# Kernel optimization log

Measured on AMD Instinct MI355X. Metric: run time of the kernel, lower is better.

The kernel has to match this reference:

```python
import jax, jax.numpy as jnp
import numpy as np

B, T, TS, J, D, H = 4, 512, 512, 17, 256, 8
CD = D // H
SCALE = CD ** -0.5


def setup_inputs() -> dict:
    key = jax.random.key(0)
    ks = jax.random.split(key, 7)
    return {
        "q": jax.random.normal(ks[0], (B, T, J, D), dtype=jnp.float32),
        "kv": jax.random.normal(ks[1], (B, TS, J, D), dtype=jnp.float32),
        "Wq": jax.random.normal(ks[2], (D, D), dtype=jnp.float32) * (D ** -0.5),
        "Wk": jax.random.normal(ks[3], (D, D), dtype=jnp.float32) * (D ** -0.5),
        "Wv": jax.random.normal(ks[4], (D, D), dtype=jnp.float32) * (D ** -0.5),
        "Wp": jax.random.normal(ks[5], (D, D), dtype=jnp.float32) * (D ** -0.5),
        "bp": jnp.zeros((D,), dtype=jnp.float32),
    }


def reference(q, kv, Wq, Wk, Wv, Wp, bp):
    b, t, j, d = q.shape
    t_sup = kv.shape[1]
    h, cd = H, CD
    # linear projections (torch Linear: x @ W^T), split heads -> [b,h,j,t,cd]
    qh = (q @ Wq.T).reshape(b, t, j, h, cd).transpose(0, 3, 2, 1, 4)
    kh = (kv @ Wk.T).reshape(b, t_sup, j, h, cd).transpose(0, 3, 2, 1, 4)
    vh = (kv @ Wv.T).reshape(b, t_sup, j, h, cd).transpose(0, 3, 2, 1, 4)
    # full attention matrix over temporal axes: [b,h,j,t,t_sup]
    scores = jnp.einsum("bhjtc,bhjsc->bhjts", qh, kh) * SCALE
    attn = jax.nn.softmax(scores, axis=-1)
    out = jnp.einsum("bhjts,bhjsc->bhjtc", attn, vh)
    out = out.transpose(0, 3, 2, 1, 4).reshape(b, t, j, d)  # [b,t,j,d]
    return out @ Wp.T + bp
```

## Files before the change

### kernel.cpp

```cpp
#include <hip/hip_runtime.h>
#include <hip/hip_bf16.h>

#define BB 4
#define TT 512
#define JJ 17
#define DD 256
#define HH 8
#define MROWS (BB*TT*JJ)
#define SZE ((size_t)MROWS * DD)
#define WSZ (DD*DD)
#define QSCALE 0.2550265247510319f
#define RST (17*256)

typedef short v8s __attribute__((ext_vector_type(8)));
typedef float v4f __attribute__((ext_vector_type(4)));
typedef float v16f __attribute__((ext_vector_type(16)));

__device__ __forceinline__ unsigned short f2bf(float f) {
    union { float f; unsigned int u; } c; c.f = f;
    unsigned int u = c.u;
    return (unsigned short)((u + 0x7FFF + ((u >> 16) & 1)) >> 16);
}
__device__ __forceinline__ unsigned int pkbf(float lo, float hi) {
    union { float f; unsigned int u; } a, b; a.f = lo; b.f = hi;
    return __builtin_amdgcn_perm(b.u + 0x8000u, a.u + 0x8000u, 0x07060302u);
}
__device__ __forceinline__ float fexp2(float x) {
    return __builtin_amdgcn_exp2f(x);
}

__device__ __forceinline__ void gld16(const unsigned short* g, unsigned short* l) {
    __builtin_amdgcn_global_load_lds(
        (const __attribute__((address_space(1))) void*)g,
        (__attribute__((address_space(3))) void*)l,
        16, 0, 0);
}

__global__ __launch_bounds__(256) void prepw_kernel(
    const float* __restrict__ Wq, const float* __restrict__ Wk,
    const float* __restrict__ Wv, const float* __restrict__ Wp,
    unsigned short* __restrict__ Wqb, unsigned short* __restrict__ Wkb,
    unsigned short* __restrict__ Wvb, unsigned short* __restrict__ Wpb)
{
    size_t k = ((size_t)blockIdx.x * 256 + threadIdx.x) * 8;
    int w = (int)(k >> 16);
    size_t off = k & (WSZ - 1);
    const float* src = (w == 0) ? Wq : (w == 1) ? Wk : (w == 2) ? Wv : Wp;
    unsigned short* dst = (w == 0) ? Wqb : (w == 1) ? Wkb : (w == 2) ? Wvb : Wpb;
    float4 x0 = *(const float4*)(src + off);
    float4 x1 = *(const float4*)(src + off + 4);
    union { unsigned short s[8]; int4 v; } u;
    u.s[0] = f2bf(x0.x); u.s[1] = f2bf(x0.y);
    u.s[2] = f2bf(x0.z); u.s[3] = f2bf(x0.w);
    u.s[4] = f2bf(x1.x); u.s[5] = f2bf(x1.y);
    u.s[6] = f2bf(x1.z); u.s[7] = f2bf(x1.w);
    *(int4*)(dst + off) = u.v;
}

__global__ __launch_bounds__(512) void gemm_kernel(
    const float* __restrict__ Aq,
    const float* __restrict__ Akv,
    const unsigned short* __restrict__ W0,
    const unsigned short* __restrict__ W1,
    const unsigned short* __restrict__ W2,
    unsigned short* __restrict__ Y0,
    unsigned short* __restrict__ Y1,
    unsigned short* __restrict__ Y2)
{
    const int z = blockIdx.y;
    const float* A          = (z == 0) ? Aq : Akv;
    const float ascale      = (z == 0) ? QSCALE : 1.f;
    const unsigned short* W = (z == 0) ? W0 : (z == 1) ? W1 : W2;
    unsigned short* Y       = (z == 0) ? Y0 : (z == 1) ? Y1 : Y2;

    const int bm = blockIdx.x;

    __shared__ unsigned short As[2][128 * 32];
    __shared__ unsigned short Bs[2][256 * 32];

    const int tid  = threadIdx.x;
    const int wv   = tid >> 6;
    const int lane = tid & 63;
    const int wm   = wv & 1;
    const int wn   = wv >> 1;
    const int quad = lane >> 4;
    const int l16  = lane & 15;

    const int srow  = tid >> 2;
    const int chunk = tid & 3;
    const int s4    = srow & 15;
    const int cg    = chunk ^ ((s4 ^ (s4 >> 2)) & 3);
    const float* gA = A + (size_t)(bm * 128 + srow) * 256 + cg * 8;
    const unsigned short* gB0 = W + (size_t)srow * 256 + cg * 8;
    const unsigned short* gB1 = W + (size_t)(128 + srow) * 256 + cg * 8;
    unsigned short* lA  = &As[0][tid * 8];
    unsigned short* lB0 = &Bs[0][tid * 8];
    unsigned short* lB1 = &Bs[0][4096 + tid * 8];

    const int rch8 = (quad ^ ((l16 ^ (l16 >> 2)) & 3)) * 8;

    v4f acc[4][4] = {};

    {
        float4 a0 = *(const float4*)(gA);
        float4 a1 = *(const float4*)(gA + 4);
        union { unsigned short s[8]; int4 v; } ua;
        ua.s[0] = f2bf(a0.x * ascale); ua.s[1] = f2bf(a0.y * ascale);
        ua.s[2] = f2bf(a0.z * ascale); ua.s[3] = f2bf(a0.w * ascale);
        ua.s[4] = f2bf(a1.x * ascale); ua.s[5] = f2bf(a1.y * ascale);
        ua.s[6] = f2bf(a1.z * ascale); ua.s[7] = f2bf(a1.w * ascale);
        *(int4*)(lA) = ua.v;
    }
    gld16(gB0, lB0);
    gld16(gB1, lB1);
    __syncthreads();

    for (int kt = 0; kt < 8; ++kt) {
        const int cur = kt & 1;
        const int nb  = cur ^ 1;
        float4 a0, a1;
        if (kt < 7) {
            const int nk = (kt + 1) * 32;
            a0 = *(const float4*)(gA + nk);
            a1 = *(const float4*)(gA + nk + 4);
            gld16(gB0 + nk, lB0 + nb * 8192);
            gld16(gB1 + nk, lB1 + nb * 8192);
        }
        v8s a[4], b[4];
        #pragma unroll
        for (int i = 0; i < 4; ++i)
            a[i] = *(const v8s*)(&As[cur][(wm * 64 + i * 16 + l16) * 32 + rch8]);
        #pragma unroll
        for (int j = 0; j < 4; ++j)
            b[j] = *(const v8s*)(&Bs[cur][(wn * 64 + j * 16 + l16) * 32 + rch8]);
        #pragma unroll
        for (int i = 0; i < 4; ++i)
            #pragma unroll
            for (int j = 0; j < 4; ++j)
                acc[i][j] = __builtin_amdgcn_mfma_f32_16x16x32_bf16(
                    a[i], b[j], acc[i][j], 0, 0, 0);
        if (kt < 7) {
            union { unsigned short s[8]; int4 v; } ua;
            ua.s[0] = f2bf(a0.x * ascale); ua.s[1] = f2bf(a0.y * ascale);
            ua.s[2] = f2bf(a0.z * ascale); ua.s[3] = f2bf(a0.w * ascale);
            ua.s[4] = f2bf(a1.x * ascale); ua.s[5] = f2bf(a1.y * ascale);
            ua.s[6] = f2bf(a1.z * ascale); ua.s[7] = f2bf(a1.w * ascale);
            *(int4*)(lA + nb * 4096) = ua.v;
        }
        __syncthreads();
    }

    #pragma unroll
    for (int i = 0; i < 4; ++i)
        #pragma unroll
        for (int j = 0; j < 4; ++j)
            #pragma unroll
            for (int r = 0; r < 4; ++r) {
                int gm = bm * 128 + wm * 64 + i * 16 + quad * 4 + r;
                int gn = wn * 64 + j * 16 + l16;
                Y[(size_t)gm * 256 + gn] = f2bf(acc[i][j][r]);
            }
}

__global__ __launch_bounds__(256) void gemmo_kernel(
    const unsigned short* __restrict__ A,
    const unsigned short* __restrict__ W,
    const float* __restrict__ bias,
    float* __restrict__ out)
{
    const int bm = blockIdx.x;

    __shared__ unsigned short As[2][64 * 32];
    __shared__ unsigned short Bs[2][256 * 32];

    const int tid  = threadIdx.x;
    const int lane = tid & 63;
    const int wn   = tid >> 6;
    const int quad = lane >> 4;
    const int l16  = lane & 15;

    const int arow  = tid >> 2;
    const int chunk = tid & 3;
    const int cgA   = (chunk ^ ((arow ^ (arow >> 2)) & 3)) * 8;
    const unsigned short* gA = A + (size_t)(bm * 64 + arow) * 256 + cgA;
    const unsigned short* gB = W + (size_t)arow * 256 + cgA;
    unsigned short* lA = &As[0][tid * 8];
    unsigned short* lB = &Bs[0][tid * 8];

    const int rch8 = (quad ^ ((l16 ^ (l16 >> 2)) & 3)) * 8;

    v4f acc[4][4] = {};

    gld16(gA, lA);
    #pragma unroll
    for (int p = 0; p < 4; ++p)
        gld16(gB + (size_t)p * 64 * 256, lB + p * 2048);
    __syncthreads();

    for (int kt = 0; kt < 8; ++kt) {
        const int cur = kt & 1;
        if (kt < 7) {
            const int nk = (kt + 1) * 32;
            const int nb = cur ^ 1;
            gld16(gA + nk, lA + nb * 2048);
            #pragma unroll
            for (int p = 0; p < 4; ++p)
                gld16(gB + (size_t)p * 64 * 256 + nk, lB + nb * 8192 + p * 2048);
        }
        v8s a[4], b[4];
        #pragma unroll
        for (int i = 0; i < 4; ++i)
            a[i] = *(const v8s*)(&As[cur][(i * 16 + l16) * 32 + rch8]);
        #pragma unroll
        for (int j = 0; j < 4; ++j)
            b[j] = *(const v8s*)(&Bs[cur][(wn * 64 + j * 16 + l16) * 32 + rch8]);
        #pragma unroll
        for (int i = 0; i < 4; ++i)
            #pragma unroll
            for (int j = 0; j < 4; ++j)
                acc[i][j] = __builtin_amdgcn_mfma_f32_16x16x32_bf16(
                    a[i], b[j], acc[i][j], 0, 0, 0);
        __syncthreads();
    }

    #pragma unroll
    for (int i = 0; i < 4; ++i)
        #pragma unroll
        for (int j = 0; j < 4; ++j)
            #pragma unroll
            for (int r = 0; r < 4; ++r) {
                int gm = bm * 64 + i * 16 + quad * 4 + r;
                int gn = wn * 64 + j * 16 + l16;
                out[(size_t)gm * 256 + gn] = acc[i][j][r] + bias[gn];
            }
}

#define VST 136

__global__ __launch_bounds__(256, 4) void attn_kernel(
    const unsigned short* __restrict__ Qp,
    const unsigned short* __restrict__ Kp,
    const unsigned short* __restrict__ Vp,
    unsigned short* __restrict__ Att)
{
    const int id  = blockIdx.x;
    const int bjh = (id & 7) | ((id >> 5) << 3);
    const int qt  = (id >> 3) & 3;
    const int h   = bjh & 7;
    const int bj  = bjh >> 3;
    const int j   = bj % 17;
    const int b_  = bj / 17;

    __shared__ unsigned short Ks[128 * 40];
    __shared__ unsigned short Vs[32 * VST];
    __shared__ float Ls[128];

    const int tid  = threadIdx.x;
    const int wave = tid >> 6;
    const int lane = tid & 63;
    const int quad = lane >> 4;
    const int l16  = lane & 15;
    const int qo   = quad & 1;
    const int q2   = quad >> 1;

    const int base0 = b_ * 512 * RST + j * 256 + h * 32;

    v8s qa[2];
    #pragma unroll
    for (int fi = 0; fi < 2; ++fi)
        qa[fi] = *(const v8s*)(
            Qp + base0 + (qt * 128 + wave * 32 + fi * 16 + l16) * RST + quad * 8);

    float lacc[2] = {0.f, 0.f};
    v16f accO = {};

    for (int kc = 0; kc < 4; ++kc) {
        __syncthreads();
        #pragma unroll
        for (int c = 0; c < 2; ++c) {
            int krow = wave * 16 + l16 + c * 64;
            *(int4*)(&Ks[krow * 40 + quad * 8]) = *(const int4*)(
                Kp + base0 + (kc * 128 + krow) * RST + quad * 8);
        }
        #pragma unroll
        for (int c = 0; c < 2; ++c) {
            int idx  = c * 256 + tid;
            int srow = idx >> 2;
            int cd0  = (idx & 3) << 3;
            int xof  = (((srow >> 3) ^ (cd0 >> 3)) << 3) + (srow & 7);
            union { int4 v; unsigned short s[8]; } u;
            u.v = *(const int4*)(
                Vp + base0 + (kc * 128 + srow) * RST + cd0);
            #pragma unroll
            for (int i = 0; i < 8; ++i)
                Vs[(cd0 + i) * VST + xof] = u.s[i];
        }
        __syncthreads();

        #pragma unroll
        for (int half = 0; half < 2; ++half) {
            #pragma unroll
            for (int si = 0; si < 4; ++si) {
                v8s kb = *(const v8s*)(&Ks[((half * 4 + si) * 16 + l16) * 40 + quad * 8]);
                v4f st0 = {}, st1 = {};
                __builtin_amdgcn_s_setprio(1);
                st0 = __builtin_amdgcn_mfma_f32_16x16x32_bf16(kb, qa[0], st0, 0, 0, 0);
                st1 = __builtin_amdgcn_mfma_f32_16x16x32_bf16(kb, qa[1], st1, 0, 0, 0);
                __builtin_amdgcn_s_setprio(0);
                float p00 = fexp2(st0[0]), p01 = fexp2(st0[1]);
                float p02 = fexp2(st0[2]), p03 = fexp2(st0[3]);
                float p10 = fexp2(st1[0]), p11 = fexp2(st1[1]);
                float p12 = fexp2(st1[2]), p13 = fexp2(st1[3]);
                lacc[0] += (p00 + p01) + (p02 + p03);
                lacc[1] += (p10 + p11) + (p12 + p13);
                unsigned int D00 = pkbf(p00, p01), D01 = pkbf(p02, p03);
                unsigned int D10 = pkbf(p10, p11), D11 = pkbf(p12, p13);
                unsigned int P0 = qo ? D00 : D10;
                unsigned int P1 = qo ? D01 : D11;
                unsigned int S0 = __shfl_xor(P0, 16);
                unsigned int S1 = __shfl_xor(P1, 16);
                union { unsigned int u[4]; v8s v; } pa;
                pa.u[0] = qo ? S0 : D00;
                pa.u[1] = qo ? S1 : D01;
                pa.u[2] = qo ? D10 : S0;
                pa.u[3] = qo ? D11 : S1;
                int cd   = qo * 16 + l16;
                int sblk = half * 8 + si * 2 + q2;
                v8s vb = *(const v8s*)(&Vs[cd * VST + ((sblk ^ (cd >> 3)) << 3)]);
                __builtin_amdgcn_s_setprio(1);
                accO = __builtin_amdgcn_mfma_f32_32x32x16_bf16(pa.v, vb, accO, 0, 0, 0);
                __builtin_amdgcn_s_setprio(0);
            }
        }
    }

    #pragma unroll
    for (int fi = 0; fi < 2; ++fi) {
        float lv = lacc[fi];
        lv += __shfl_xor(lv, 16);
        lv += __shfl_xor(lv, 32);
        if (quad == 0) Ls[wave * 32 + fi * 16 + l16] = lv;
    }
    asm volatile("s_waitcnt lgkmcnt(0)" ::: "memory");

    const int cdo = qo * 16 + l16;
    #pragma unroll
    for (int g = 0; g < 4; ++g) {
        float4 lv = *(float4*)(&Ls[wave * 32 + g * 8 + q2 * 4]);
        float rl[4] = {1.f / lv.x, 1.f / lv.y, 1.f / lv.z, 1.f / lv.w};
        #pragma unroll
        for (int r = 0; r < 4; ++r) {
            int qrow = g * 8 + q2 * 4 + r;
            int trow = qt * 128 + wave * 32 + qrow;
            float v  = accO[g * 4 + r] * rl[r];
            Att[(size_t)(base0 + trow * RST + cdo)] = f2bf(v);
        }
    }
}

extern "C" void kernel_launch(void* const* d_in, const int* in_sizes, int n_in,
                              void* d_out, int out_size, void* d_ws, size_t ws_size,
                              hipStream_t stream) {
    const float* q  = (const float*)d_in[0];
    const float* kv = (const float*)d_in[1];
    const float* Wq = (const float*)d_in[2];
    const float* Wk = (const float*)d_in[3];
    const float* Wv = (const float*)d_in[4];
    const float* Wp = (const float*)d_in[5];
    const float* bp = (const float*)d_in[6];

    unsigned short* ws  = (unsigned short*)d_ws;
    unsigned short* Qp  = ws;
    unsigned short* Kp  = ws + SZE;
    unsigned short* Vp  = ws + 2 * SZE;
    unsigned short* Att = ws + 3 * SZE;
    unsigned short* Wqb = ws + 4 * SZE;
    unsigned short* Wkb = Wqb + WSZ;
    unsigned short* Wvb = Wkb + WSZ;
    unsigned short* Wpb = Wvb + WSZ;
    float* out = (float*)d_out;

    prepw_kernel<<<128, 256, 0, stream>>>(Wq, Wk, Wv, Wp,
                                          Wqb, Wkb, Wvb, Wpb);
    gemm_kernel<<<dim3(272, 3), 512, 0, stream>>>(
        q, kv, Wqb, Wkb, Wvb, Qp, Kp, Vp);
    attn_kernel<<<dim3(2176), 256, 0, stream>>>(Qp, Kp, Vp, Att);
    gemmo_kernel<<<dim3(544), 256, 0, stream>>>(Att, Wpb, bp, out);
}
```

Baseline: 198.6 us.

## Drop LDS staging in projection GEMMs and load MFMA operands directly from global

Both projection GEMM kernels stop staging tiles through double-buffered shared memory with async global-to-LDS loads and barriers. Each wave now reads its MFMA operand fragments straight from global memory, relying on the L1/L2 caches for reuse across waves. The QKV GEMM also shrinks to 64-row tiles with 256 threads, doubling the grid. This removes LDS traffic and synchronisation but gives up explicit prefetch and adds redundant global/cache reads, since the A rows are now loaded by all four waves and converted four times.

```diff
diff --git a/kernel.cpp b/kernel.cpp
--- a/kernel.cpp
+++ b/kernel.cpp
@@ -27,13 +27,6 @@
 }
 __device__ __forceinline__ float fexp2(float x) {
     return __builtin_amdgcn_exp2f(x);
-}
-
-__device__ __forceinline__ void gld16(const unsigned short* g, unsigned short* l) {
-    __builtin_amdgcn_global_load_lds(
-        (const __attribute__((address_space(1))) void*)g,
-        (__attribute__((address_space(3))) void*)l,
-        16, 0, 0);
 }
 
 __global__ __launch_bounds__(256) void prepw_kernel(
@@ -57,7 +50,7 @@
     *(int4*)(dst + off) = u.v;
 }
 
-__global__ __launch_bounds__(512) void gemm_kernel(
+__global__ __launch_bounds__(256) void gemm_kernel(
     const float* __restrict__ Aq,
     const float* __restrict__ Akv,
     const unsigned short* __restrict__ W0,
@@ -73,81 +66,42 @@
     const unsigned short* W = (z == 0) ? W0 : (z == 1) ? W1 : W2;
     unsigned short* Y       = (z == 0) ? Y0 : (z == 1) ? Y1 : Y2;
 
-    const int bm = blockIdx.x;
-
-    __shared__ unsigned short As[2][128 * 32];
-    __shared__ unsigned short Bs[2][256 * 32];
-
+    const int bm   = blockIdx.x;
     const int tid  = threadIdx.x;
-    const int wv   = tid >> 6;
+    const int wn   = tid >> 6;
     const int lane = tid & 63;
-    const int wm   = wv & 1;
-    const int wn   = wv >> 1;
     const int quad = lane >> 4;
     const int l16  = lane & 15;
 
-    const int srow  = tid >> 2;
-    const int chunk = tid & 3;
-    const int s4    = srow & 15;
-    const int cg    = chunk ^ ((s4 ^ (s4 >> 2)) & 3);
-    const float* gA = A + (size_t)(bm * 128 + srow) * 256 + cg * 8;
-    const unsigned short* gB0 = W + (size_t)srow * 256 + cg * 8;
-    const unsigned short* gB1 = W + (size_t)(128 + srow) * 256 + cg * 8;
-    unsigned short* lA  = &As[0][tid * 8];
-    unsigned short* lB0 = &Bs[0][tid * 8];
-    unsigned short* lB1 = &Bs[0][4096 + tid * 8];
-
-    const int rch8 = (quad ^ ((l16 ^ (l16 >> 2)) & 3)) * 8;
+    const float*          ga = A + (size_t)(bm * 64 + l16) * 256 + quad * 8;
+    const unsigned short* gb = W + (size_t)(wn * 64 + l16) * 256 + quad * 8;
 
     v4f acc[4][4] = {};
 
-    {
-        float4 a0 = *(const float4*)(gA);
-        float4 a1 = *(const float4*)(gA + 4);
-        union { unsigned short s[8]; int4 v; } ua;
-        ua.s[0] = f2bf(a0.x * ascale); ua.s[1] = f2bf(a0.y * ascale);
-        ua.s[2] = f2bf(a0.z * ascale); ua.s[3] = f2bf(a0.w * ascale);
-        ua.s[4] = f2bf(a1.x * ascale); ua.s[5] = f2bf(a1.y * ascale);
-        ua.s[6] = f2bf(a1.z * ascale); ua.s[7] = f2bf(a1.w * ascale);
-        *(int4*)(lA) = ua.v;
-    }
-    gld16(gB0, lB0);
-    gld16(gB1, lB1);
-    __syncthreads();
-
+    #pragma unroll 2
     for (int kt = 0; kt < 8; ++kt) {
-        const int cur = kt & 1;
-        const int nb  = cur ^ 1;
-        float4 a0, a1;
-        if (kt < 7) {
-            const int nk = (kt + 1) * 32;
-            a0 = *(const float4*)(gA + nk);
-            a1 = *(const float4*)(gA + nk + 4);
-            gld16(gB0 + nk, lB0 + nb * 8192);
-            gld16(gB1 + nk, lB1 + nb * 8192);
-        }
+        const int k0 = kt * 32;
         v8s a[4], b[4];
         #pragma unroll
-        for (int i = 0; i < 4; ++i)
-            a[i] = *(const v8s*)(&As[cur][(wm * 64 + i * 16 + l16) * 32 + rch8]);
+        for (int i = 0; i < 4; ++i) {
+            float4 x0 = *(const float4*)(ga + i * 16 * 256 + k0);
+            float4 x1 = *(const float4*)(ga + i * 16 * 256 + k0 + 4);
+            union { unsigned short s[8]; v8s v; } ua;
+            ua.s[0] = f2bf(x0.x * ascale); ua.s[1] = f2bf(x0.y * ascale);
+            ua.s[2] = f2bf(x0.z * ascale); ua.s[3] = f2bf(x0.w * ascale);
+            ua.s[4] = f2bf(x1.x * ascale); ua.s[5] = f2bf(x1.y * ascale);
+            ua.s[6] = f2bf(x1.z * ascale); ua.s[7] = f2bf(x1.w * ascale);
+            a[i] = ua.v;
+        }
         #pragma unroll
         for (int j = 0; j < 4; ++j)
-            b[j] = *(const v8s*)(&Bs[cur][(wn * 64 + j * 16 + l16) * 32 + rch8]);
+            b[j] = *(const v8s*)(gb + (size_t)j * 16 * 256 + k0);
         #pragma unroll
         for (int i = 0; i < 4; ++i)
             #pragma unroll
             for (int j = 0; j < 4; ++j)
                 acc[i][j] = __builtin_amdgcn_mfma_f32_16x16x32_bf16(
                     a[i], b[j], acc[i][j], 0, 0, 0);
-        if (kt < 7) {
-            union { unsigned short s[8]; int4 v; } ua;
-            ua.s[0] = f2bf(a0.x * ascale); ua.s[1] = f2bf(a0.y * ascale);
-            ua.s[2] = f2bf(a0.z * ascale); ua.s[3] = f2bf(a0.w * ascale);
-            ua.s[4] = f2bf(a1.x * ascale); ua.s[5] = f2bf(a1.y * ascale);
-            ua.s[6] = f2bf(a1.z * ascale); ua.s[7] = f2bf(a1.w * ascale);
-            *(int4*)(lA + nb * 4096) = ua.v;
-        }
-        __syncthreads();
     }
 
     #pragma unroll
@@ -156,7 +110,7 @@
         for (int j = 0; j < 4; ++j)
             #pragma unroll
             for (int r = 0; r < 4; ++r) {
-                int gm = bm * 128 + wm * 64 + i * 16 + quad * 4 + r;
+                int gm = bm * 64 + i * 16 + quad * 4 + r;
                 int gn = wn * 64 + j * 16 + l16;
                 Y[(size_t)gm * 256 + gn] = f2bf(acc[i][j][r]);
             }
@@ -168,59 +122,34 @@
     const float* __restrict__ bias,
     float* __restrict__ out)
 {
-    const int bm = blockIdx.x;
-
-    __shared__ unsigned short As[2][64 * 32];
-    __shared__ unsigned short Bs[2][256 * 32];
-
+    const int bm   = blockIdx.x;
     const int tid  = threadIdx.x;
+    const int wn   = tid >> 6;
     const int lane = tid & 63;
-    const int wn   = tid >> 6;
     const int quad = lane >> 4;
     const int l16  = lane & 15;
 
-    const int arow  = tid >> 2;
-    const int chunk = tid & 3;
-    const int cgA   = (chunk ^ ((arow ^ (arow >> 2)) & 3)) * 8;
-    const unsigned short* gA = A + (size_t)(bm * 64 + arow) * 256 + cgA;
-    const unsigned short* gB = W + (size_t)arow * 256 + cgA;
-    unsigned short* lA = &As[0][tid * 8];
-    unsigned short* lB = &Bs[0][tid * 8];
-
-    const int rch8 = (quad ^ ((l16 ^ (l16 >> 2)) & 3)) * 8;
+    const unsigned short* ga = A + (size_t)(bm * 64 + l16) * 256 + quad * 8;
+    const unsigned short* gb = W + (size_t)(wn * 64 + l16) * 256 + quad * 8;
 
     v4f acc[4][4] = {};
 
-    gld16(gA, lA);
-    #pragma unroll
-    for (int p = 0; p < 4; ++p)
-        gld16(gB + (size_t)p * 64 * 256, lB + p * 2048);
-    __syncthreads();
-
+    #pragma unroll 2
     for (int kt = 0; kt < 8; ++kt) {
-        const int cur = kt & 1;
-        if (kt < 7) {
-            const int nk = (kt + 1) * 32;
-            const int nb = cur ^ 1;
-            gld16(gA + nk, lA + nb * 2048);
-            #pragma unroll
-            for (int p = 0; p < 4; ++p)
-                gld16(gB + (size_t)p * 64 * 256 + nk, lB + nb * 8192 + p * 2048);
-        }
+        const int k0 = kt * 32;
         v8s a[4], b[4];
         #pragma unroll
         for (int i = 0; i < 4; ++i)
-            a[i] = *(const v8s*)(&As[cur][(i * 16 + l16) * 32 + rch8]);
+            a[i] = *(const v8s*)(ga + (size_t)i * 16 * 256 + k0);
         #pragma unroll
         for (int j = 0; j < 4; ++j)
-            b[j] = *(const v8s*)(&Bs[cur][(wn * 64 + j * 16 + l16) * 32 + rch8]);
+            b[j] = *(const v8s*)(gb + (size_t)j * 16 * 256 + k0);
         #pragma unroll
         for (int i = 0; i < 4; ++i)
             #pragma unroll
             for (int j = 0; j < 4; ++j)
                 acc[i][j] = __builtin_amdgcn_mfma_f32_16x16x32_bf16(
                     a[i], b[j], acc[i][j], 0, 0, 0);
-        __syncthreads();
     }
 
     #pragma unroll
@@ -382,7 +311,7 @@
 
     prepw_kernel<<<128, 256, 0, stream>>>(Wq, Wk, Wv, Wp,
                                           Wqb, Wkb, Wvb, Wpb);
-    gemm_kernel<<<dim3(272, 3), 512, 0, stream>>>(
+    gemm_kernel<<<dim3(544, 3), 256, 0, stream>>>(
         q, kv, Wqb, Wkb, Wvb, Qp, Kp, Vp);
     attn_kernel<<<dim3(2176), 256, 0, stream>>>(Qp, Kp, Vp, Att);
     gemmo_kernel<<<dim3(544), 256, 0, stream>>>(Att, Wpb, bp, out);
```

Measured after the change: 269.3 us. 1.36x slower.
